# Kernel tuning notes

Measured on AMD Instinct MI355X. Metric: run time of the kernel, lower is better.

Reference implementation:

```python
import jax, jax.numpy as jnp
import numpy as np

B = 262144      # batch
DIN = 100       # input covariate dim (cfg_density[0][0])
H = 64          # hidden dim
G = 10          # num_grid -> density output dim G+1
NH = 5          # number of dosage-bucket heads in Multi_head


def setup_inputs() -> dict:
    key = jax.random.key(0)
    ks = jax.random.split(key, 16)
    s = 0.05
    return {
        "dosage": jax.random.uniform(ks[0], (B,), dtype=jnp.float32),
        "x": jax.random.normal(ks[1], (B, DIN), dtype=jnp.float32),
        # density feature MLP (two Linear+ReLU layers)
        "dW0": jax.random.normal(ks[2], (DIN, H), dtype=jnp.float32) * s,
        "db0": jax.random.normal(ks[3], (H,), dtype=jnp.float32) * s,
        "dW1": jax.random.normal(ks[4], (H, H), dtype=jnp.float32) * s,
        "db1": jax.random.normal(ks[5], (H,), dtype=jnp.float32) * s,
        # Density_Block: Linear(H -> G+1) then softmax + grid interpolation
        "dbW": jax.random.normal(ks[6], (H, G + 1), dtype=jnp.float32) * s,
        "dbB": jax.random.normal(ks[7], (G + 1,), dtype=jnp.float32) * s,
        # Multi_head: 5 structurally identical heads, params stacked on axis 0
        # layer0: Treat_Linear(64 -> 64, relu, istreat=1)
        "W0": jax.random.normal(ks[8], (NH, H, H), dtype=jnp.float32) * s,
        "tw0": jax.random.normal(ks[9], (NH, H), dtype=jnp.float32) * s,
        "b0": jax.random.normal(ks[10], (NH, H), dtype=jnp.float32) * s,
        # layer1 (last): Treat_Linear(64 -> 1, no act, istreat=1)
        "W1": jax.random.normal(ks[11], (NH, H, 1), dtype=jnp.float32) * s,
        "tw1": jax.random.normal(ks[12], (NH, 1), dtype=jnp.float32) * s,
        "b1": jax.random.normal(ks[13], (NH, 1), dtype=jnp.float32) * s,
    }


def reference(dosage, x, dW0, db0, dW1, db1, dbW, dbB, W0, tw0, b0, W1, tw1, b1):
    # hidden feature MLP
    hidden = jax.nn.relu(x @ dW0 + db0)
    hidden = jax.nn.relu(hidden @ dW1 + db1)            # [B, H]

    # ---- Density_Block: softmax over grid, dual gather + linear interpolation
    p = jax.nn.softmax(hidden @ dbW + dbB, axis=1)      # [B, G+1]
    tB = dosage * G
    U = jnp.ceil(tB)
    inter = 1.0 - (U - tB)                              # fractional position in cell
    Ui = U.astype(jnp.int32)
    Li = Ui - 1
    Li = Li + (Li < 0).astype(jnp.int32)                # clamp L=-1 -> 0
    pL = jnp.take_along_axis(p, Li[:, None], axis=1)[:, 0]
    pU = jnp.take_along_axis(p, Ui[:, None], axis=1)[:, 0]
    g = pL + (pU - pL) * inter                          # [B]

    # ---- Multi_head: 5 heads on dosage buckets [0,.2),[.2,.4),...,[.8,1.)
    t = dosage
    # layer0: out = feat @ W + t * tw + b, relu; compute all heads, select later
    h0 = jax.nn.relu(
        jnp.einsum('bi,hio->bho', hidden, W0)
        + t[:, None, None] * tw0[None]
        + b0[None]
    )                                                   # [B, NH, H]
    # last layer: no activation
    out1 = (jnp.einsum('bho,hoj->bhj', h0, W1)
            + t[:, None, None] * tw1[None]
            + b1[None])                                 # [B, NH, 1]
    bucket = jnp.clip(jnp.floor(t * NH).astype(jnp.int32), 0, NH - 1)
    Q = jnp.take_along_axis(out1, bucket[:, None, None], axis=1)[:, 0, :]  # [B, 1]
    return g, Q
```

## Files before the change

### kernel.cpp

```cpp
#include <hip/hip_runtime.h>

typedef __attribute__((ext_vector_type(8))) short  short8;
typedef __attribute__((ext_vector_type(4))) float  floatx4;
typedef __attribute__((ext_vector_type(4))) int    intx4;

constexpr int DIN = 100;
constexpr int H   = 64;
constexpr int G   = 10;
constexpr int NH  = 5;
constexpr int MWG = 128;
constexpr int HP  = 72;

constexpr int NF_DW0 = 16, NF_DW1 = 8, NF_DBW = 2;
constexpr int NF_LIN = NF_DW0 + NF_DW1 + NF_DBW;
constexpr int NF_TOT = NF_LIN + 40;

__device__ __forceinline__ unsigned short f2bf_rne(float f) {
    union { float f; unsigned u; } v{f};
    unsigned r = v.u + 0x7FFF + ((v.u >> 16) & 1);
    return (unsigned short)(r >> 16);
}

__device__ __forceinline__ short8 pack8(const float* f) {
    intx4 p;
    #pragma unroll
    for (int j = 0; j < 4; ++j) {
        unsigned a = __float_as_uint(f[2 * j])     + 0x8000u;
        unsigned b = __float_as_uint(f[2 * j + 1]) + 0x8000u;
        p[j] = (int)((b & 0xFFFF0000u) | (a >> 16));
    }
    union { intx4 i; short8 s; } u; u.i = p;
    return u.s;
}

__device__ __forceinline__ unsigned short f2bf_hu(float f) {
    return (unsigned short)((__float_as_uint(f) + 0x8000u) >> 16);
}

__device__ __forceinline__ short8 ldfrag(const unsigned short* __restrict__ ws,
                                         int f, int lane) {
    return *(const short8*)(ws + (size_t)(f * 64 + lane) * 8);
}

__global__ __launch_bounds__(64) void pack_kernel(
    const float* __restrict__ dW0, const float* __restrict__ dW1,
    const float* __restrict__ dbW, const float* __restrict__ W0,
    unsigned short* __restrict__ ws)
{
    const int f = blockIdx.x;
    const int lane = threadIdx.x;
    const int q = lane >> 4, cl = lane & 15;
    float v[8];
    if (f < NF_DW0) {
        int c = f >> 2, g = f & 3;
        #pragma unroll
        for (int j = 0; j < 8; ++j) {
            int k = c * 32 + q * 8 + j, n = g * 16 + cl;
            v[j] = (k < DIN) ? dW0[k * H + n] : 0.0f;
        }
    } else if (f < NF_DW0 + NF_DW1) {
        int r = f - NF_DW0; int c = r >> 2, g = r & 3;
        #pragma unroll
        for (int j = 0; j < 8; ++j) {
            int k = c * 32 + q * 8 + j, n = g * 16 + cl;
            v[j] = dW1[k * H + n];
        }
    } else if (f < NF_LIN) {
        int c = f - (NF_DW0 + NF_DW1);
        #pragma unroll
        for (int j = 0; j < 8; ++j) {
            int k = c * 32 + q * 8 + j, n = cl;
            v[j] = (n <= G) ? dbW[k * (G + 1) + n] : 0.0f;
        }
    } else {
        int r = f - NF_LIN; int h = r >> 3; r &= 7; int c = r >> 2, g = r & 3;
        #pragma unroll
        for (int j = 0; j < 8; ++j) {
            int k = c * 32 + q * 8 + j, n = g * 16 + cl;
            v[j] = W0[(h * H + k) * H + n];
        }
    }
    short8 s;
    #pragma unroll
    for (int j = 0; j < 8; ++j) s[j] = (short)f2bf_rne(v[j]);
    *(short8*)(ws + (size_t)(f * 64 + lane) * 8) = s;
}

__global__ __launch_bounds__(256, 4) void drnet_mfma(
    const float* __restrict__ dosage, const float* __restrict__ x,
    const float* __restrict__ db0, const float* __restrict__ db1,
    const float* __restrict__ dbB,
    const float* __restrict__ tw0, const float* __restrict__ b0,
    const float* __restrict__ W1, const float* __restrict__ tw1,
    const float* __restrict__ b1,
    const unsigned short* __restrict__ wsfrag,
    float* __restrict__ outg, float* __restrict__ outq)
{
    __shared__ unsigned short hbuf[MWG * HP];
    const int tid  = threadIdx.x;
    const int wave = tid >> 6, lane = tid & 63;
    const int q = lane >> 4, cl = lane & 15;
    const int rowbase = blockIdx.x * MWG + wave * 32;
    unsigned short* hb = hbuf + wave * 32 * HP;

    float t8[2][4];
    int   bk8[2][4];
    #pragma unroll
    for (int mt = 0; mt < 2; ++mt) {
        floatx4 tv = *(const floatx4*)(dosage + rowbase + mt * 16 + 4 * q);
        #pragma unroll
        for (int r = 0; r < 4; ++r) {
            float t = tv[r];
            t8[mt][r] = t;
            int bk = (int)floorf(t * (float)NH);
            bk8[mt][r] = min(max(bk, 0), NH - 1);
        }
    }

    #pragma unroll 1
    for (int mt = 0; mt < 2; ++mt) {
        short8 a1[4];
        const float* xr = x + (size_t)(rowbase + mt * 16 + cl) * DIN;
        #pragma unroll
        for (int cch = 0; cch < 4; ++cch) {
            float f[8];
            if (cch < 3) {
                floatx4 u0 = *(const floatx4*)(xr + cch * 32 + q * 8);
                floatx4 u1 = *(const floatx4*)(xr + cch * 32 + q * 8 + 4);
                f[0]=u0.x; f[1]=u0.y; f[2]=u0.z; f[3]=u0.w;
                f[4]=u1.x; f[5]=u1.y; f[6]=u1.z; f[7]=u1.w;
            } else {
                if (q == 0) {
                    floatx4 u0 = *(const floatx4*)(xr + 96);
                    f[0]=u0.x; f[1]=u0.y; f[2]=u0.z; f[3]=u0.w;
                    f[4]=f[5]=f[6]=f[7]=0.0f;
                } else {
                    #pragma unroll
                    for (int j = 0; j < 8; ++j) f[j] = 0.0f;
                }
            }
            a1[cch] = pack8(f);
        }
        floatx4 acc[4];
        #pragma unroll
        for (int g = 0; g < 4; ++g) acc[g] = (floatx4)0.0f;
        #pragma unroll
        for (int cch = 0; cch < 4; ++cch)
            #pragma unroll
            for (int g = 0; g < 4; ++g) {
                short8 bf = ldfrag(wsfrag, cch * 4 + g, lane);
                acc[g] = __builtin_amdgcn_mfma_f32_16x16x32_bf16(a1[cch], bf, acc[g], 0, 0, 0);
            }
        #pragma unroll
        for (int g = 0; g < 4; ++g) {
            float bias = db0[g * 16 + cl];
            #pragma unroll
            for (int r = 0; r < 4; ++r)
                hb[(mt * 16 + 4 * q + r) * HP + g * 16 + cl] =
                    f2bf_hu(fmaxf(acc[g][r] + bias, 0.0f));
        }
    }

    #pragma unroll 1
    for (int mt = 0; mt < 2; ++mt) {
        short8 a2[2];
        #pragma unroll
        for (int cch = 0; cch < 2; ++cch)
            a2[cch] = *(const short8*)(hb + (mt * 16 + cl) * HP + cch * 32 + q * 8);
        floatx4 acc[4];
        #pragma unroll
        for (int g = 0; g < 4; ++g) acc[g] = (floatx4)0.0f;
        #pragma unroll
        for (int cch = 0; cch < 2; ++cch)
            #pragma unroll
            for (int g = 0; g < 4; ++g) {
                short8 bf = ldfrag(wsfrag, NF_DW0 + cch * 4 + g, lane);
                acc[g] = __builtin_amdgcn_mfma_f32_16x16x32_bf16(a2[cch], bf, acc[g], 0, 0, 0);
            }
        #pragma unroll
        for (int g = 0; g < 4; ++g) {
            float bias = db1[g * 16 + cl];
            #pragma unroll
            for (int r = 0; r < 4; ++r)
                hb[(mt * 16 + 4 * q + r) * HP + g * 16 + cl] =
                    f2bf_hu(fmaxf(acc[g][r] + bias, 0.0f));
        }
    }

    short8 af[2][2];
    #pragma unroll
    for (int mt = 0; mt < 2; ++mt)
        #pragma unroll
        for (int cch = 0; cch < 2; ++cch)
            af[mt][cch] = *(const short8*)(hb + (mt * 16 + cl) * HP + cch * 32 + q * 8);

    {
        floatx4 accd[2];
        accd[0] = (floatx4)0.0f; accd[1] = (floatx4)0.0f;
        #pragma unroll
        for (int cch = 0; cch < 2; ++cch) {
            short8 bf = ldfrag(wsfrag, NF_DW0 + NF_DW1 + cch, lane);
            #pragma unroll
            for (int mt = 0; mt < 2; ++mt)
                accd[mt] = __builtin_amdgcn_mfma_f32_16x16x32_bf16(af[mt][cch], bf, accd[mt], 0, 0, 0);
        }
        const float dbBv = (cl <= G) ? dbB[cl] : 0.0f;
        #pragma unroll
        for (int mt = 0; mt < 2; ++mt) {
            float gout[4];
            #pragma unroll
            for (int r = 0; r < 4; ++r) {
                float e = (cl <= G) ? __expf(accd[mt][r] + dbBv) : 0.0f;
                float s = e;
                s += __shfl_xor(s, 1); s += __shfl_xor(s, 2);
                s += __shfl_xor(s, 4); s += __shfl_xor(s, 8);
                const float t  = t8[mt][r];
                const float tB = t * (float)G;
                const float U  = ceilf(tB);
                const float inter = 1.0f - (U - tB);
                int Ui = (int)U; int Li = Ui - 1; if (Li < 0) Li = 0;
                float pL = __shfl(e, q * 16 + Li);
                float pU = __shfl(e, q * 16 + Ui);
                gout[r] = (pL + (pU - pL) * inter) / s;
            }
            if (cl == 0) {
                floatx4 gv = { gout[0], gout[1], gout[2], gout[3] };
                *(floatx4*)(outg + rowbase + mt * 16 + 4 * q) = gv;
            }
        }
    }

    float qp[2][4] = {{0,0,0,0},{0,0,0,0}};
    #pragma unroll 1
    for (int h = 0; h < NH; ++h) {
        #pragma unroll
        for (int gh = 0; gh < 2; ++gh) {
            floatx4 acch[2][2];
            #pragma unroll
            for (int mt = 0; mt < 2; ++mt)
                #pragma unroll
                for (int g = 0; g < 2; ++g) acch[mt][g] = (floatx4)0.0f;
            #pragma unroll
            for (int cch = 0; cch < 2; ++cch)
                #pragma unroll
                for (int g = 0; g < 2; ++g) {
                    short8 bf = ldfrag(wsfrag, NF_LIN + h * 8 + cch * 4 + gh * 2 + g, lane);
                    #pragma unroll
                    for (int mt = 0; mt < 2; ++mt)
                        acch[mt][g] = __builtin_amdgcn_mfma_f32_16x16x32_bf16(af[mt][cch], bf, acch[mt][g], 0, 0, 0);
                }
            #pragma unroll
            for (int g = 0; g < 2; ++g) {
                const int off = h * H + (gh * 2 + g) * 16 + cl;
                const float tw0v = tw0[off], b0v = b0[off], w1v = W1[off];
                #pragma unroll
                for (int mt = 0; mt < 2; ++mt)
                    #pragma unroll
                    for (int r = 0; r < 4; ++r) {
                        float h0 = acch[mt][g][r] + t8[mt][r] * tw0v + b0v;
                        float c  = fmaxf(h0, 0.0f) * w1v;
                        qp[mt][r] += (bk8[mt][r] == h) ? c : 0.0f;
                    }
            }
        }
    }
    #pragma unroll
    for (int mt = 0; mt < 2; ++mt) {
        #pragma unroll
        for (int r = 0; r < 4; ++r) {
            float s = qp[mt][r];
            s += __shfl_xor(s, 1); s += __shfl_xor(s, 2);
            s += __shfl_xor(s, 4); s += __shfl_xor(s, 8);
            const int h = bk8[mt][r];
            qp[mt][r] = s + t8[mt][r] * tw1[h] + b1[h];
        }
        if (cl == 0) {
            floatx4 Qv = { qp[mt][0], qp[mt][1], qp[mt][2], qp[mt][3] };
            *(floatx4*)(outq + rowbase + mt * 16 + 4 * q) = Qv;
        }
    }
}

extern "C" void kernel_launch(void* const* d_in, const int* in_sizes, int n_in,
                              void* d_out, int out_size, void* d_ws, size_t ws_size,
                              hipStream_t stream) {
    const float* dosage = (const float*)d_in[0];
    const float* x      = (const float*)d_in[1];
    const float* dW0    = (const float*)d_in[2];
    const float* db0    = (const float*)d_in[3];
    const float* dW1    = (const float*)d_in[4];
    const float* db1    = (const float*)d_in[5];
    const float* dbW    = (const float*)d_in[6];
    const float* dbB    = (const float*)d_in[7];
    const float* W0     = (const float*)d_in[8];
    const float* tw0    = (const float*)d_in[9];
    const float* b0     = (const float*)d_in[10];
    const float* W1     = (const float*)d_in[11];
    const float* tw1    = (const float*)d_in[12];
    const float* b1     = (const float*)d_in[13];

    const int Btot = in_sizes[0];
    float* outg = (float*)d_out;
    float* outq = outg + Btot;
    unsigned short* ws = (unsigned short*)d_ws;

    pack_kernel<<<NF_TOT, 64, 0, stream>>>(dW0, dW1, dbW, W0, ws);
    drnet_mfma<<<Btot / MWG, 256, 0, stream>>>(dosage, x, db0, db1, dbB,
                                               tw0, b0, W1, tw1, b1,
                                               ws, outg, outq);
}
```

Before: 201.5 us.

## Sort rows by dosage bucket per block to skip unneeded head computations

Builds a per-block histogram and counting-sort permutation of the 128 rows by head bucket in shared memory. Each 16-row MFMA tile then gathers its hidden rows from LDS and evaluates only the heads spanned by that tile, instead of all five heads for every row. Q results are scattered back through shared memory and written out in row order. This adds atomics, several block barriers and gather traffic in exchange for roughly a fivefold cut in head MFMA work.

Measured after the change: 211.1 us. 1.05x slower.

```diff
diff --git a/kernel.cpp b/kernel.cpp
--- a/kernel.cpp
+++ b/kernel.cpp
@@ -97,12 +97,21 @@
     float* __restrict__ outg, float* __restrict__ outq)
 {
     __shared__ unsigned short hbuf[MWG * HP];
+    __shared__ int            perm[MWG];
+    __shared__ float          tbuf[MWG];
+    __shared__ unsigned char  bkbuf[MWG];
+    __shared__ float          qbuf[MWG];
+    __shared__ int            hist[NH];
+    __shared__ int            offs[NH];
+
     const int tid  = threadIdx.x;
     const int wave = tid >> 6, lane = tid & 63;
     const int q = lane >> 4, cl = lane & 15;
     const int rowbase = blockIdx.x * MWG + wave * 32;
     unsigned short* hb = hbuf + wave * 32 * HP;
 
+    if (tid < NH) hist[tid] = 0;
+
     float t8[2][4];
     int   bk8[2][4];
     #pragma unroll
@@ -115,6 +124,14 @@
             int bk = (int)floorf(t * (float)NH);
             bk8[mt][r] = min(max(bk, 0), NH - 1);
         }
+    }
+    __syncthreads();
+    if (cl == 0) {
+        #pragma unroll
+        for (int mt = 0; mt < 2; ++mt)
+            #pragma unroll
+            for (int r = 0; r < 4; ++r)
+                atomicAdd(&hist[bk8[mt][r]], 1);
     }
 
     #pragma unroll 1
@@ -230,54 +247,78 @@
         }
     }
 
-    float qp[2][4] = {{0,0,0,0},{0,0,0,0}};
+    __syncthreads();
+    if (tid == 0) {
+        int a = 0;
+        #pragma unroll
+        for (int h = 0; h < NH; ++h) { offs[h] = a; a += hist[h]; }
+    }
+    __syncthreads();
+    if (cl == 0) {
+        #pragma unroll
+        for (int mt = 0; mt < 2; ++mt)
+            #pragma unroll
+            for (int r = 0; r < 4; ++r) {
+                const int bk  = bk8[mt][r];
+                const int pos = atomicAdd(&offs[bk], 1);
+                perm[pos]  = wave * 32 + mt * 16 + 4 * q + r;
+                tbuf[pos]  = t8[mt][r];
+                bkbuf[pos] = (unsigned char)bk;
+            }
+    }
+    __syncthreads();
+
     #pragma unroll 1
-    for (int h = 0; h < NH; ++h) {
-        #pragma unroll
-        for (int gh = 0; gh < 2; ++gh) {
-            floatx4 acch[2][2];
-            #pragma unroll
-            for (int mt = 0; mt < 2; ++mt)
-                #pragma unroll
-                for (int g = 0; g < 2; ++g) acch[mt][g] = (floatx4)0.0f;
+    for (int mt = 0; mt < 2; ++mt) {
+        const int base = (wave * 2 + mt) * 16;
+        const int prow = perm[base + cl];
+        short8 ag[2];
+        ag[0] = *(const short8*)(hbuf + prow * HP + q * 8);
+        ag[1] = *(const short8*)(hbuf + prow * HP + 32 + q * 8);
+        floatx4 tv = *(const floatx4*)(tbuf + base + 4 * q);
+        const unsigned bku = *(const unsigned*)(bkbuf + base + 4 * q);
+        const int blo = bkbuf[base], bhi = bkbuf[base + 15];
+        float qp4[4] = {0.0f, 0.0f, 0.0f, 0.0f};
+        #pragma unroll 1
+        for (int h = blo; h <= bhi; ++h) {
+            floatx4 acch[4];
+            #pragma unroll
+            for (int g = 0; g < 4; ++g) acch[g] = (floatx4)0.0f;
             #pragma unroll
             for (int cch = 0; cch < 2; ++cch)
                 #pragma unroll
-                for (int g = 0; g < 2; ++g) {
-                    short8 bf = ldfrag(wsfrag, NF_LIN + h * 8 + cch * 4 + gh * 2 + g, lane);
-                    #pragma unroll
-                    for (int mt = 0; mt < 2; ++mt)
-                        acch[mt][g] = __builtin_amdgcn_mfma_f32_16x16x32_bf16(af[mt][cch], bf, acch[mt][g], 0, 0, 0);
+                for (int g = 0; g < 4; ++g) {
+                    short8 bf = ldfrag(wsfrag, NF_LIN + h * 8 + cch * 4 + g, lane);
+                    acch[g] = __builtin_amdgcn_mfma_f32_16x16x32_bf16(ag[cch], bf, acch[g], 0, 0, 0);
                 }
             #pragma unroll
-            for (int g = 0; g < 2; ++g) {
-                const int off = h * H + (gh * 2 + g) * 16 + cl;
+            for (int g = 0; g < 4; ++g) {
+                const int off = h * H + g * 16 + cl;
                 const float tw0v = tw0[off], b0v = b0[off], w1v = W1[off];
                 #pragma unroll
-                for (int mt = 0; mt < 2; ++mt)
-                    #pragma unroll
-                    for (int r = 0; r < 4; ++r) {
-                        float h0 = acch[mt][g][r] + t8[mt][r] * tw0v + b0v;
-                        float c  = fmaxf(h0, 0.0f) * w1v;
-                        qp[mt][r] += (bk8[mt][r] == h) ? c : 0.0f;
-                    }
-            }
-        }
-    }
-    #pragma unroll
-    for (int mt = 0; mt < 2; ++mt) {
+                for (int r = 0; r < 4; ++r) {
+                    float h0 = acch[g][r] + tv[r] * tw0v + b0v;
+                    float c  = fmaxf(h0, 0.0f) * w1v;
+                    qp4[r] += (((bku >> (8 * r)) & 0xFFu) == (unsigned)h) ? c : 0.0f;
+                }
+            }
+        }
         #pragma unroll
         for (int r = 0; r < 4; ++r) {
-            float s = qp[mt][r];
+            float s = qp4[r];
             s += __shfl_xor(s, 1); s += __shfl_xor(s, 2);
             s += __shfl_xor(s, 4); s += __shfl_xor(s, 8);
-            const int h = bk8[mt][r];
-            qp[mt][r] = s + t8[mt][r] * tw1[h] + b1[h];
-        }
-        if (cl == 0) {
-            floatx4 Qv = { qp[mt][0], qp[mt][1], qp[mt][2], qp[mt][3] };
-            *(floatx4*)(outq + rowbase + mt * 16 + 4 * q) = Qv;
-        }
+            if (cl == 0) {
+                const int bk = (int)((bku >> (8 * r)) & 0xFFu);
+                qbuf[perm[base + 4 * q + r]] = s + tv[r] * tw1[bk] + b1[bk];
+            }
+        }
+    }
+
+    __syncthreads();
+    if (tid < MWG / 4) {
+        floatx4 v = *(const floatx4*)(qbuf + tid * 4);
+        *(floatx4*)(outq + blockIdx.x * MWG + tid * 4) = v;
     }
 }
 
```
